# Performance work log

Hardware: AMD Instinct MI355X
Metric: run time of the kernel (lower is better)

The kernel has to match this reference:

```python
import jax, jax.numpy as jnp
import numpy as np

B, S, D, H, E, F, K = 4, 1024, 1024, 16, 8, 4096, 2
HD = D // H  # 64
EPS = 1e-6


def _rmsnorm(x, w):
    return x * jax.lax.rsqrt(jnp.mean(x * x, axis=-1, keepdims=True) + EPS) * w


def _rope(x, cos, sin):
    # x: [B,S,H,HD]; cos/sin: [S,HD//2]
    b, s, h, hd = x.shape
    x2 = x.reshape(b, s, h, hd // 2, 2)
    xr, xi = x2[..., 0], x2[..., 1]
    c = cos[None, :, None, :]
    sn = sin[None, :, None, :]
    or_ = xr * c - xi * sn
    oi = xr * sn + xi * c
    return jnp.stack([or_, oi], axis=-1).reshape(b, s, h, hd)


def setup_inputs() -> dict:
    key = jax.random.key(0)
    ks = jax.random.split(key, 16)
    sc = 0.02
    # rotary tables (standard LLaMa rope)
    inv = 1.0 / (10000.0 ** (np.arange(0, HD, 2, dtype=np.float32) / HD))
    ang = np.outer(np.arange(S, dtype=np.float32), inv)
    return {
        "q": jax.random.normal(ks[0], (B, S, D), jnp.float32),
        "k": jax.random.normal(ks[1], (B, S, D), jnp.float32),
        "v": jax.random.normal(ks[2], (B, S, D), jnp.float32),
        "freqs_cos": jnp.asarray(np.cos(ang)),
        "freqs_sin": jnp.asarray(np.sin(ang)),
        "att_norm_w": jnp.ones((D,), jnp.float32),
        "ffn_norm_w": jnp.ones((D,), jnp.float32),
        "wq": jax.random.normal(ks[3], (D, D), jnp.float32) * sc,
        "wk": jax.random.normal(ks[4], (D, D), jnp.float32) * sc,
        "wv": jax.random.normal(ks[5], (D, D), jnp.float32) * sc,
        "wo": jax.random.normal(ks[6], (D, D), jnp.float32) * sc,
        "router_w": jax.random.normal(ks[7], (E, D), jnp.float32) * sc,
        "router_b": jnp.zeros((E,), jnp.float32),
        "w1": jax.random.normal(ks[8], (E, F, D), jnp.float32) * sc,
        "w2": jax.random.normal(ks[9], (E, D, F), jnp.float32) * sc,
        "w3": jax.random.normal(ks[10], (E, F, D), jnp.float32) * sc,
        "is_causal": 1,
    }


def _attention(qn, kn, vn, freqs_cos, freqs_sin, wq, wk, wv, wo, is_causal):
    b, s, d = qn.shape
    qh = (qn @ wq.T).reshape(b, s, H, HD)
    kh = (kn @ wk.T).reshape(b, s, H, HD)
    vh = (vn @ wv.T).reshape(b, s, H, HD)
    qh = _rope(qh, freqs_cos, freqs_sin)
    kh = _rope(kh, freqs_cos, freqs_sin)
    scores = jnp.einsum("bqhd,bkhd->bhqk", qh, kh) / jnp.sqrt(jnp.float32(HD))
    if is_causal:
        causal = jnp.tril(jnp.ones((s, s), bool))
        scores = jnp.where(causal[None, None], scores, jnp.float32(-1e30))
    probs = jax.nn.softmax(scores, axis=-1)
    out = jnp.einsum("bhqk,bkhd->bqhd", probs, vh).reshape(b, s, d)
    return out @ wo.T


def _sparse_moe(x, router_w, router_b, w1, w2, w3):
    # x: [B,S,D]
    flat = x.reshape(-1, x.shape[-1])  # [T,D]
    logits = flat @ router_w.T + router_b  # [T,E]
    top_v, top_i = jax.lax.top_k(logits, K)  # eval mode: no noise
    probs = jax.nn.softmax(top_v, axis=-1)  # softmax over -inf-filled == softmax over top-k
    gates = jnp.sum(jax.nn.one_hot(top_i, E, dtype=flat.dtype) * probs[..., None], axis=1)  # [T,E]
    y = jnp.zeros_like(flat)
    for e in range(E):  # fixed small expert loop; gate==0 for unselected tokens (faithful to masked dispatch)
        hgate = jax.nn.silu(flat @ w1[e].T) * (flat @ w3[e].T)  # SwiGLU FFN_LLaMa
        y = y + gates[:, e : e + 1] * (hgate @ w2[e].T)
    return y.reshape(x.shape)


def reference(q, k, v, freqs_cos, freqs_sin, att_norm_w, ffn_norm_w, wq, wk, wv, wo,
              router_w, router_b, w1, w2, w3, is_causal):
    qn = _rmsnorm(q, att_norm_w)
    # self-attention path: k = v = normed q (q.clone())
    h = q + _attention(qn, qn, qn, freqs_cos, freqs_sin, wq, wk, wv, wo, is_causal)
    out = h + _sparse_moe(_rmsnorm(h, ffn_norm_w), router_w, router_b, w1, w2, w3)
    return out
```

## Files before the change

kernel.cpp:

```cpp
#include <hip/hip_runtime.h>
#include <hip/hip_bf16.h>
#include <math.h>

#define NB 4
#define SQ 1024
#define DM 1024
#define NH 16
#define HDm 64
#define NE 8
#define FFd 4096
#define NTOK 4096
#define RTOT 9216
#define EPSF 1e-6f

typedef __attribute__((ext_vector_type(8))) short bf16x8_t;
typedef __attribute__((ext_vector_type(4))) float f32x4_t;
typedef const __attribute__((address_space(1))) void* gas_t;
typedef __attribute__((address_space(3))) void* las_t;

__device__ __forceinline__ float b2f(unsigned short u){
  return __uint_as_float(((unsigned int)u) << 16);
}
__device__ __forceinline__ unsigned short f2b(float f){
  __hip_bfloat16 h = __float2bfloat16(f);
  unsigned short u;
  __builtin_memcpy(&u, &h, 2);
  return u;
}

__global__ __launch_bounds__(256) void convert_k(const float* __restrict__ s,
                                                 unsigned short* __restrict__ d, int n4){
  int i = blockIdx.x*256 + threadIdx.x;
  if (i >= n4) return;
  float4 v = ((const float4*)s)[i];
  ushort4 o; o.x=f2b(v.x); o.y=f2b(v.y); o.z=f2b(v.z); o.w=f2b(v.w);
  ((ushort4*)d)[i] = o;
}

__global__ __launch_bounds__(256) void split_k(const float* __restrict__ s,
                                               unsigned short* __restrict__ hi,
                                               unsigned short* __restrict__ lo, int n4){
  int i = blockIdx.x*256 + threadIdx.x;
  if (i >= n4) return;
  float4 v = ((const float4*)s)[i];
  ushort4 h, l;
  h.x=f2b(v.x); l.x=f2b(v.x - b2f(h.x));
  h.y=f2b(v.y); l.y=f2b(v.y - b2f(h.y));
  h.z=f2b(v.z); l.z=f2b(v.z - b2f(h.z));
  h.w=f2b(v.w); l.w=f2b(v.w - b2f(h.w));
  ((ushort4*)hi)[i] = h;
  ((ushort4*)lo)[i] = l;
}

__global__ __launch_bounds__(256) void rmsnorm_k(const float* __restrict__ x,
                                                 const float* __restrict__ w,
                                                 float* __restrict__ o){
  int row = blockIdx.x; int t = threadIdx.x;
  float4 v = ((const float4*)(x + (size_t)row*DM))[t];
  float ss = v.x*v.x + v.y*v.y + v.z*v.z + v.w*v.w;
  #pragma unroll
  for (int d=32; d; d>>=1) ss += __shfl_down(ss, d, 64);
  __shared__ float red[4];
  int wid = t>>6, ln = t&63;
  if (ln==0) red[wid] = ss;
  __syncthreads();
  float tot = red[0]+red[1]+red[2]+red[3];
  float sc = 1.0f/sqrtf(tot*(1.0f/DM) + EPSF);
  float4 wv = ((const float4*)w)[t];
  float4 ov = { v.x*sc*wv.x, v.y*sc*wv.y, v.z*sc*wv.z, v.w*sc*wv.w };
  ((float4*)(o + (size_t)row*DM))[t] = ov;
}

__global__ __launch_bounds__(256) void rmsnorm_split_k(const float* __restrict__ x,
                                                       const float* __restrict__ w,
                                                       unsigned short* __restrict__ hi,
                                                       unsigned short* __restrict__ lo){
  int row = blockIdx.x; int t = threadIdx.x;
  float4 v = ((const float4*)(x + (size_t)row*DM))[t];
  float ss = v.x*v.x + v.y*v.y + v.z*v.z + v.w*v.w;
  #pragma unroll
  for (int d=32; d; d>>=1) ss += __shfl_down(ss, d, 64);
  __shared__ float red[4];
  int wid = t>>6, ln = t&63;
  if (ln==0) red[wid] = ss;
  __syncthreads();
  float tot = red[0]+red[1]+red[2]+red[3];
  float sc = 1.0f/sqrtf(tot*(1.0f/DM) + EPSF);
  float4 wv = ((const float4*)w)[t];
  float4 ov = { v.x*sc*wv.x, v.y*sc*wv.y, v.z*sc*wv.z, v.w*sc*wv.w };
  ushort4 h, l;
  h.x=f2b(ov.x); l.x=f2b(ov.x - b2f(h.x));
  h.y=f2b(ov.y); l.y=f2b(ov.y - b2f(h.y));
  h.z=f2b(ov.z); l.z=f2b(ov.z - b2f(h.z));
  h.w=f2b(ov.w); l.w=f2b(ov.w - b2f(h.w));
  ((ushort4*)(hi + (size_t)row*DM))[t] = h;
  ((ushort4*)(lo + (size_t)row*DM))[t] = l;
}

__global__ __launch_bounds__(256) void gemm_nt_split(
  const unsigned short* __restrict__ Ah, const unsigned short* __restrict__ Al,
  const unsigned short* __restrict__ Bh0, const unsigned short* __restrict__ Bl0,
  const unsigned short* __restrict__ Bh1, const unsigned short* __restrict__ Bl1,
  const unsigned short* __restrict__ Bh2, const unsigned short* __restrict__ Bl2,
  float* __restrict__ C0, float* __restrict__ C1, float* __restrict__ C2,
  const float* __restrict__ resid, int Kd, int Ncols)
{
  const unsigned short* Bh = (blockIdx.z==0)?Bh0:(blockIdx.z==1)?Bh1:Bh2;
  const unsigned short* Bl = (blockIdx.z==0)?Bl0:(blockIdx.z==1)?Bl1:Bl2;
  float* C = (blockIdx.z==0)?C0:(blockIdx.z==1)?C1:C2;
  __shared__ unsigned short AsH[128*32];
  __shared__ unsigned short AsL[128*32];
  __shared__ unsigned short BsH[128*32];
  __shared__ unsigned short BsL[128*32];
  const int t = threadIdx.x;
  const int w = t>>6, lane = t&63;
  const int wm = w>>1, wn = w&1;
  const int lm = lane&15, fk = (lane>>4)*8;
  const int row0 = blockIdx.y*128, col0 = blockIdx.x*128;
  f32x4_t acc[4][4];
  #pragma unroll
  for (int i=0;i<4;i++)
    #pragma unroll
    for (int j=0;j<4;j++){ f32x4_t z = {0.f,0.f,0.f,0.f}; acc[i][j]=z; }
  for (int k0=0;k0<Kd;k0+=32){
    __syncthreads();
    #pragma unroll
    for (int j=0;j<2;j++){
      const int chunk = j*4 + w;
      const int gt = chunk*64 + lane;
      const int rw_ = gt>>2, kp = (gt&3)*8;
      const size_t aoff = (size_t)(row0+rw_)*Kd + k0 + kp;
      const size_t boff = (size_t)(col0+rw_)*Kd + k0 + kp;
      __builtin_amdgcn_global_load_lds((gas_t)(Ah + aoff), (las_t)(AsH + chunk*512), 16, 0, 0);
      __builtin_amdgcn_global_load_lds((gas_t)(Al + aoff), (las_t)(AsL + chunk*512), 16, 0, 0);
      __builtin_amdgcn_global_load_lds((gas_t)(Bh + boff), (las_t)(BsH + chunk*512), 16, 0, 0);
      __builtin_amdgcn_global_load_lds((gas_t)(Bl + boff), (las_t)(BsL + chunk*512), 16, 0, 0);
    }
    __syncthreads();
    bf16x8_t ah[4], al[4], bh[4], bl[4];
    #pragma unroll
    for (int f=0;f<4;f++){
      const size_t ao = (size_t)(wm*64 + f*16 + lm)*32 + fk;
      const size_t bo = (size_t)(wn*64 + f*16 + lm)*32 + fk;
      ah[f] = *(const bf16x8_t*)(AsH + ao);
      al[f] = *(const bf16x8_t*)(AsL + ao);
      bh[f] = *(const bf16x8_t*)(BsH + bo);
      bl[f] = *(const bf16x8_t*)(BsL + bo);
    }
    #pragma unroll
    for (int i=0;i<4;i++)
      #pragma unroll
      for (int j=0;j<4;j++){
        acc[i][j] = __builtin_amdgcn_mfma_f32_16x16x32_bf16(ah[i], bh[j], acc[i][j], 0, 0, 0);
        acc[i][j] = __builtin_amdgcn_mfma_f32_16x16x32_bf16(al[i], bh[j], acc[i][j], 0, 0, 0);
        acc[i][j] = __builtin_amdgcn_mfma_f32_16x16x32_bf16(ah[i], bl[j], acc[i][j], 0, 0, 0);
      }
  }
  const int rbase = row0 + wm*64 + (lane>>4)*4;
  const int cbase = col0 + wn*64 + lm;
  #pragma unroll
  for (int i=0;i<4;i++)
    #pragma unroll
    for (int j=0;j<4;j++)
      #pragma unroll
      for (int r=0;r<4;r++){
        const size_t idx = (size_t)(rbase + i*16 + r)*Ncols + cbase + j*16;
        float v = acc[i][j][r];
        if (resid) v += resid[idx];
        C[idx] = v;
      }
}

__global__ __launch_bounds__(256) void rope_k(float* __restrict__ qh, float* __restrict__ kh,
  const float* __restrict__ fc, const float* __restrict__ fs){
  int idx = blockIdx.x*256 + threadIdx.x;
  if (idx >= NTOK*NH*32) return;
  int i = idx & 31;
  int h = (idx>>5) & (NH-1);
  int n = idx >> 9;
  int s = n & (SQ-1);
  float c = fc[s*32+i], sn = fs[s*32+i];
  size_t base = (size_t)n*DM + h*HDm + 2*i;
  float xr = qh[base], xi = qh[base+1];
  qh[base]   = xr*c - xi*sn;
  qh[base+1] = xr*sn + xi*c;
  xr = kh[base]; xi = kh[base+1];
  kh[base]   = xr*c - xi*sn;
  kh[base+1] = xr*sn + xi*c;
}

__global__ __launch_bounds__(256) void flash_k(
  const float* __restrict__ qh, const float* __restrict__ kh, const float* __restrict__ vh,
  float* __restrict__ ctx, const int* __restrict__ causp)
{
  __shared__ float Qt[64][68];
  __shared__ float KP[64][68];
  __shared__ float Vs[64][68];
  __shared__ float red[64][17];
  __shared__ float mrow[64], lrow[64], arow[64];
  const int qt = blockIdx.x;
  const int b = blockIdx.y >> 4, h = blockIdx.y & 15;
  const int t = threadIdx.x;
  const int row = t>>2, cb = (t&3)*16;
  const int ty = t>>4, tx = t&15;
  const size_t headoff = ((size_t)b*SQ)*DM + (size_t)h*HDm;
  const int q0 = qt*64;
  {
    const float* qp = qh + headoff + (size_t)(q0+row)*DM + cb;
    #pragma unroll
    for (int j=0;j<4;j++){
      float4 v = *(const float4*)(qp + 4*j);
      Qt[cb+4*j+0][row]=v.x; Qt[cb+4*j+1][row]=v.y; Qt[cb+4*j+2][row]=v.z; Qt[cb+4*j+3][row]=v.w;
    }
  }
  if (t<64){ mrow[t]=-1e30f; lrow[t]=0.f; }
  float O[4][4] = {};
  const int causal = *causp;
  const int ktmax = causal ? qt : (SQ/64 - 1);
  for (int kt=0; kt<=ktmax; ++kt){
    const int k0 = kt*64;
    __syncthreads();
    {
      const float* kp_ = kh + headoff + (size_t)(k0+row)*DM + cb;
      const float* vp_ = vh + headoff + (size_t)(k0+row)*DM + cb;
      #pragma unroll
      for (int j=0;j<4;j++){
        float4 v = *(const float4*)(kp_ + 4*j);
        KP[cb+4*j+0][row]=v.x; KP[cb+4*j+1][row]=v.y; KP[cb+4*j+2][row]=v.z; KP[cb+4*j+3][row]=v.w;
        float4 u = *(const float4*)(vp_ + 4*j);
        *(float4*)&Vs[row][cb+4*j] = u;
      }
    }
    __syncthreads();
    float Sv[4][4] = {};
    #pragma unroll 16
    for (int kk=0;kk<64;kk++){
      float4 qa = *(const float4*)&Qt[kk][ty*4];
      float4 kb = *(const float4*)&KP[kk][tx*4];
      float a4[4]={qa.x,qa.y,qa.z,qa.w}, b4[4]={kb.x,kb.y,kb.z,kb.w};
      #pragma unroll
      for (int i=0;i<4;i++)
        #pragma unroll
        for (int j=0;j<4;j++)
          Sv[i][j] = fmaf(a4[i], b4[j], Sv[i][j]);
    }
    #pragma unroll
    for (int i=0;i<4;i++){
      float lm = -3.0e30f;
      #pragma unroll
      for (int j=0;j<4;j++){
        float s = Sv[i][j]*0.125f;
        if (causal && (k0+tx*4+j) > (q0+ty*4+i)) s = -1e30f;
        Sv[i][j] = s;
        lm = fmaxf(lm, s);
      }
      red[ty*4+i][tx] = lm;
    }
    __syncthreads();
    if (t<64){
      float m = red[t][0];
      #pragma unroll
      for (int j=1;j<16;j++) m = fmaxf(m, red[t][j]);
      float mo = mrow[t];
      float mn = fmaxf(mo, m);
      float al = expf(mo - mn);
      mrow[t]=mn; arow[t]=al; lrow[t]*=al;
    }
    __syncthreads();
    #pragma unroll
    for (int i=0;i<4;i++){
      int r = ty*4+i;
      float mn = mrow[r];
      float rs = 0.f;
      #pragma unroll
      for (int j=0;j<4;j++){
        float p = expf(Sv[i][j]-mn);
        KP[tx*4+j][r] = p;
        rs += p;
      }
      red[r][tx] = rs;
    }
    __syncthreads();
    if (t<64){
      float s_=0.f;
      #pragma unroll
      for (int j=0;j<16;j++) s_ += red[t][j];
      lrow[t] += s_;
    }
    #pragma unroll
    for (int i=0;i<4;i++){
      float al = arow[ty*4+i];
      #pragma unroll
      for (int j=0;j<4;j++) O[i][j]*=al;
    }
    #pragma unroll 16
    for (int kk=0;kk<64;kk++){
      float4 pa = *(const float4*)&KP[kk][ty*4];
      float4 vb = *(const float4*)&Vs[kk][tx*4];
      float a4[4]={pa.x,pa.y,pa.z,pa.w}, b4[4]={vb.x,vb.y,vb.z,vb.w};
      #pragma unroll
      for (int i=0;i<4;i++)
        #pragma unroll
        for (int j=0;j<4;j++)
          O[i][j] = fmaf(a4[i], b4[j], O[i][j]);
    }
  }
  __syncthreads();
  #pragma unroll
  for (int i=0;i<4;i++){
    float il = 1.0f/lrow[ty*4+i];
    float4 ov = { O[i][0]*il, O[i][1]*il, O[i][2]*il, O[i][3]*il };
    *(float4*)(ctx + headoff + (size_t)(q0+ty*4+i)*DM + tx*4) = ov;
  }
}

__global__ __launch_bounds__(256) void router_k(
  const float* __restrict__ hn, const float* __restrict__ rw, const float* __restrict__ rb,
  int* __restrict__ topi, float* __restrict__ topp, int* __restrict__ counts)
{
  const int n = blockIdx.x, t = threadIdx.x;
  float4 x = ((const float4*)(hn + (size_t)n*DM))[t];
  float p[NE];
  #pragma unroll
  for (int e=0;e<NE;e++){
    float4 wv = ((const float4*)(rw + (size_t)e*DM))[t];
    p[e] = x.x*wv.x + x.y*wv.y + x.z*wv.z + x.w*wv.w;
  }
  #pragma unroll
  for (int e=0;e<NE;e++)
    #pragma unroll
    for (int d=32; d; d>>=1) p[e] += __shfl_down(p[e], d, 64);
  __shared__ float red[4][NE];
  int wid=t>>6, ln=t&63;
  if (ln==0){
    #pragma unroll
    for (int e=0;e<NE;e++) red[wid][e]=p[e];
  }
  __syncthreads();
  if (t==0){
    float v1=-3e30f, v2=-3e30f; int i1=0, i2=0;
    for (int e=0;e<NE;e++){
      float v = red[0][e]+red[1][e]+red[2][e]+red[3][e]+rb[e];
      if (v > v1){ v2=v1;i2=i1; v1=v;i1=e; }
      else if (v > v2){ v2=v;i2=e; }
    }
    float ex = expf(v2-v1);
    float g1 = 1.0f/(1.0f+ex);
    float g2 = ex*g1;
    topi[2*n]=i1; topi[2*n+1]=i2;
    topp[2*n]=g1; topp[2*n+1]=g2;
    atomicAdd(&counts[i1],1); atomicAdd(&counts[i2],1);
  }
}

__global__ void offsets_k(const int* __restrict__ counts, int* __restrict__ offs){
  if (blockIdx.x==0 && threadIdx.x==0){
    int run=0;
    for (int e=0;e<NE;e++){ offs[e]=run; run += (counts[e]+127)&~127; }
    offs[NE]=run;
  }
}

__global__ __launch_bounds__(256) void assign_k(const int* __restrict__ topi,
  const int* __restrict__ offs, int* __restrict__ cursor,
  int* __restrict__ list, int* __restrict__ inv){
  int t = blockIdx.x*256 + threadIdx.x;
  if (t >= NTOK*2) return;
  int e = topi[t];
  int slot = atomicAdd(&cursor[e], 1);
  int pos = offs[e] + slot;
  list[pos] = t>>1;
  inv[t] = pos;
}

__global__ __launch_bounds__(256) void gather_k(const float* __restrict__ hn,
  const int* __restrict__ offs, const int* __restrict__ counts, const int* __restrict__ list,
  unsigned short* __restrict__ xg){
  const int p = blockIdx.x;
  if (p >= offs[NE]) return;
  int e=0;
  while (offs[e+1] <= p) ++e;
  const int t = threadIdx.x;
  ushort4 o;
  if (p - offs[e] < counts[e]){
    int n = list[p];
    float4 x = ((const float4*)(hn + (size_t)n*DM))[t];
    o.x=f2b(x.x); o.y=f2b(x.y); o.z=f2b(x.z); o.w=f2b(x.w);
  } else { o.x=0; o.y=0; o.z=0; o.w=0; }
  ((ushort4*)(xg + (size_t)p*DM))[t] = o;
}

__global__ __launch_bounds__(256) void gemm_moe_bf16(
  const unsigned short* __restrict__ Aall, const unsigned short* __restrict__ Wall,
  unsigned short* __restrict__ Call, const int* __restrict__ offs, int Kd, int Ncols)
{
  const int row0 = blockIdx.y*128;
  if (row0 >= offs[NE]) return;
  int e=0;
  while (offs[e+1] <= row0) ++e;
  const unsigned short* Wp = Wall + (size_t)e*Ncols*Kd;
  const int col0 = blockIdx.x*128;
  __shared__ unsigned short As[128*32];
  __shared__ unsigned short Bs[128*32];
  const int t = threadIdx.x;
  const int w = t>>6, lane = t&63;
  const int wm = w>>1, wn = w&1;
  const int lm = lane&15, fk = (lane>>4)*8;
  f32x4_t acc[4][4];
  #pragma unroll
  for (int i=0;i<4;i++)
    #pragma unroll
    for (int j=0;j<4;j++){ f32x4_t z = {0.f,0.f,0.f,0.f}; acc[i][j]=z; }
  for (int k0=0;k0<Kd;k0+=32){
    __syncthreads();
    #pragma unroll
    for (int j=0;j<2;j++){
      const int chunk = j*4 + w;
      const int gt = chunk*64 + lane;
      const int rw_ = gt>>2, kp = (gt&3)*8;
      __builtin_amdgcn_global_load_lds((gas_t)(Aall + (size_t)(row0+rw_)*Kd + k0 + kp),
                                       (las_t)(As + chunk*512), 16, 0, 0);
      __builtin_amdgcn_global_load_lds((gas_t)(Wp + (size_t)(col0+rw_)*Kd + k0 + kp),
                                       (las_t)(Bs + chunk*512), 16, 0, 0);
    }
    __syncthreads();
    bf16x8_t af[4], bfr[4];
    #pragma unroll
    for (int f=0;f<4;f++){
      af[f]  = *(const bf16x8_t*)(As + (size_t)(wm*64 + f*16 + lm)*32 + fk);
      bfr[f] = *(const bf16x8_t*)(Bs + (size_t)(wn*64 + f*16 + lm)*32 + fk);
    }
    #pragma unroll
    for (int i=0;i<4;i++)
      #pragma unroll
      for (int j=0;j<4;j++)
        acc[i][j] = __builtin_amdgcn_mfma_f32_16x16x32_bf16(af[i], bfr[j], acc[i][j], 0, 0, 0);
  }
  const int rbase = row0 + wm*64 + (lane>>4)*4;
  const int cbase = col0 + wn*64 + lm;
  #pragma unroll
  for (int i=0;i<4;i++)
    #pragma unroll
    for (int j=0;j<4;j++)
      #pragma unroll
      for (int r=0;r<4;r++)
        Call[(size_t)(rbase + i*16 + r)*Ncols + cbase + j*16] = f2b(acc[i][j][r]);
}

__global__ __launch_bounds__(256) void silu_mul_k(unsigned short* __restrict__ h1,
                                                  const unsigned short* __restrict__ h3){
  size_t i = (size_t)blockIdx.x*256 + threadIdx.x;
  ushort4 a = ((const ushort4*)h1)[i];
  ushort4 b = ((const ushort4*)h3)[i];
  ushort4 o;
  float fa, fb, s_;
  fa=b2f(a.x); fb=b2f(b.x); s_=fa/(1.f+__expf(-fa)); o.x=f2b(s_*fb);
  fa=b2f(a.y); fb=b2f(b.y); s_=fa/(1.f+__expf(-fa)); o.y=f2b(s_*fb);
  fa=b2f(a.z); fb=b2f(b.z); s_=fa/(1.f+__expf(-fa)); o.z=f2b(s_*fb);
  fa=b2f(a.w); fb=b2f(b.w); s_=fa/(1.f+__expf(-fa)); o.w=f2b(s_*fb);
  ((ushort4*)h1)[i] = o;
}

__global__ __launch_bounds__(256) void combine_k(const float* __restrict__ h,
  const unsigned short* __restrict__ yb, const float* __restrict__ topp,
  const int* __restrict__ inv, float* __restrict__ out)
{
  const int n = blockIdx.x, t = threadIdx.x;
  const int p0 = inv[2*n], p1 = inv[2*n+1];
  const float g0 = topp[2*n], g1 = topp[2*n+1];
  float4 hv = ((const float4*)(h + (size_t)n*DM))[t];
  ushort4 y0 = ((const ushort4*)(yb + (size_t)p0*DM))[t];
  ushort4 y1 = ((const ushort4*)(yb + (size_t)p1*DM))[t];
  float4 ov;
  ov.x = hv.x + g0*b2f(y0.x) + g1*b2f(y1.x);
  ov.y = hv.y + g0*b2f(y0.y) + g1*b2f(y1.y);
  ov.z = hv.z + g0*b2f(y0.z) + g1*b2f(y1.z);
  ov.w = hv.w + g0*b2f(y0.w) + g1*b2f(y1.w);
  ((float4*)(out + (size_t)n*DM))[t] = ov;
}

extern "C" void kernel_launch(void* const* d_in, const int* in_sizes, int n_in,
                              void* d_out, int out_size, void* d_ws, size_t ws_size,
                              hipStream_t stream)
{
  (void)in_sizes; (void)n_in; (void)out_size; (void)ws_size;
  const float* q    = (const float*)d_in[0];
  const float* fc   = (const float*)d_in[3];
  const float* fs   = (const float*)d_in[4];
  const float* attw = (const float*)d_in[5];
  const float* ffnw = (const float*)d_in[6];
  const float* wq   = (const float*)d_in[7];
  const float* wk   = (const float*)d_in[8];
  const float* wv   = (const float*)d_in[9];
  const float* wo   = (const float*)d_in[10];
  const float* rw   = (const float*)d_in[11];
  const float* rb   = (const float*)d_in[12];
  const float* w1   = (const float*)d_in[13];
  const float* w2   = (const float*)d_in[14];
  const float* w3   = (const float*)d_in[15];
  const int*   caus = (const int*)d_in[16];
  float* out = (float*)d_out;

  char* ws = (char*)d_ws;
  size_t off = 0;
  auto take = [&](size_t bytes)->char*{ char* r = ws + off; off += (bytes + 255) & ~(size_t)255; return r; };
  unsigned short* qnh = (unsigned short*)take((size_t)NTOK*DM*2);
  unsigned short* qnl = (unsigned short*)take((size_t)NTOK*DM*2);
  float* qh   = (float*)take((size_t)NTOK*DM*4);
  float* kh   = (float*)take((size_t)NTOK*DM*4);
  float* vh   = (float*)take((size_t)NTOK*DM*4);
  float* hbuf = (float*)take((size_t)NTOK*DM*4);
  unsigned short* h1  = (unsigned short*)take((size_t)RTOT*FFd*2);
  unsigned short* h3  = (unsigned short*)take((size_t)RTOT*FFd*2);
  unsigned short* yb  = (unsigned short*)take((size_t)RTOT*DM*2);
  unsigned short* w1b = (unsigned short*)take((size_t)NE*FFd*DM*2);
  unsigned short* w3b = (unsigned short*)take((size_t)NE*FFd*DM*2);
  unsigned short* w2b = (unsigned short*)take((size_t)NE*FFd*DM*2);
  int*   counts = (int*)take(64);
  int*   cursor = counts + 8;
  int*   offs   = (int*)take(64);
  int*   topi   = (int*)take((size_t)NTOK*2*4);
  float* topp   = (float*)take((size_t)NTOK*2*4);
  int*   list   = (int*)take((size_t)RTOT*4);
  int*   inv    = (int*)take((size_t)NTOK*2*4);

  float* ctx = (float*)qnh;
  unsigned short* ctxh = (unsigned short*)qh;
  unsigned short* ctxl = ctxh + (size_t)NTOK*DM;
  float* hn = kh;
  unsigned short* xg = yb;
  unsigned short* wqh = (unsigned short*)h1;
  unsigned short* wql = wqh + (size_t)DM*DM;
  unsigned short* wkh = wql + (size_t)DM*DM;
  unsigned short* wkl = wkh + (size_t)DM*DM;
  unsigned short* wvh = wkl + (size_t)DM*DM;
  unsigned short* wvl = wvh + (size_t)DM*DM;
  unsigned short* woh = wvl + (size_t)DM*DM;
  unsigned short* wol = woh + (size_t)DM*DM;

  const int nw4 = NE*FFd*DM/4;
  convert_k<<<nw4/256, 256, 0, stream>>>(w1, w1b, nw4);
  convert_k<<<nw4/256, 256, 0, stream>>>(w3, w3b, nw4);
  convert_k<<<nw4/256, 256, 0, stream>>>(w2, w2b, nw4);

  const int nwq4 = DM*DM/4;
  split_k<<<nwq4/256, 256, 0, stream>>>(wq, wqh, wql, nwq4);
  split_k<<<nwq4/256, 256, 0, stream>>>(wk, wkh, wkl, nwq4);
  split_k<<<nwq4/256, 256, 0, stream>>>(wv, wvh, wvl, nwq4);
  split_k<<<nwq4/256, 256, 0, stream>>>(wo, woh, wol, nwq4);

  rmsnorm_split_k<<<NTOK, 256, 0, stream>>>(q, attw, qnh, qnl);
  gemm_nt_split<<<dim3(8,32,3), 256, 0, stream>>>(qnh, qnl,
      wqh, wql, wkh, wkl, wvh, wvl, qh, kh, vh, nullptr, DM, DM);
  rope_k<<<NTOK*NH*32/256, 256, 0, stream>>>(qh, kh, fc, fs);
  flash_k<<<dim3(SQ/64, NB*NH), 256, 0, stream>>>(qh, kh, vh, ctx, caus);
  split_k<<<NTOK*DM/4/256, 256, 0, stream>>>(ctx, ctxh, ctxl, NTOK*DM/4);
  gemm_nt_split<<<dim3(8,32,1), 256, 0, stream>>>(ctxh, ctxl,
      woh, wol, woh, wol, woh, wol, hbuf, hbuf, hbuf, q, DM, DM);
  rmsnorm_k<<<NTOK, 256, 0, stream>>>(hbuf, ffnw, hn);

  hipMemsetAsync(counts, 0, 64, stream);
  router_k<<<NTOK, 256, 0, stream>>>(hn, rw, rb, topi, topp, counts);
  offsets_k<<<1, 64, 0, stream>>>(counts, offs);
  assign_k<<<NTOK*2/256, 256, 0, stream>>>(topi, offs, cursor, list, inv);
  gather_k<<<RTOT, 256, 0, stream>>>(hn, offs, counts, list, xg);

  gemm_moe_bf16<<<dim3(FFd/128, RTOT/128), 256, 0, stream>>>(xg, w1b, h1, offs, DM, FFd);
  gemm_moe_bf16<<<dim3(FFd/128, RTOT/128), 256, 0, stream>>>(xg, w3b, h3, offs, DM, FFd);
  silu_mul_k<<<RTOT*FFd/4/256, 256, 0, stream>>>(h1, h3);
  gemm_moe_bf16<<<dim3(DM/128, RTOT/128), 256, 0, stream>>>(h1, w2b, yb, offs, FFd, DM);
  combine_k<<<NTOK, 256, 0, stream>>>(hbuf, yb, topp, inv, out);
}
```

Before: 1.415 ms.

## Rewrite flash attention with bf16 MFMA and fuse split into epilogue

Replaces the scalar fp32 flash-attention kernel with a bf16 MFMA version. RoPE now writes pre-scaled bf16 Q and K, and a new kernel transposes V into bf16. The attention kernel loads tiles into LDS with global_load_lds, keeps softmax stats in registers with lane shuffles instead of shared-memory reductions, and writes the hi/lo bf16 split of ctx directly, so the separate split kernel is removed. This trades fp32 attention accuracy for bf16 inputs and P, and adds an extra V transpose pass.

```diff
diff --git a/kernel.cpp b/kernel.cpp
--- a/kernel.cpp
+++ b/kernel.cpp
@@ -171,8 +171,9 @@
       }
 }
 
-__global__ __launch_bounds__(256) void rope_k(float* __restrict__ qh, float* __restrict__ kh,
-  const float* __restrict__ fc, const float* __restrict__ fs){
+__global__ __launch_bounds__(256) void rope_bf16_k(const float* __restrict__ qh,
+  const float* __restrict__ kh, const float* __restrict__ fc, const float* __restrict__ fs,
+  unsigned short* __restrict__ qb, unsigned short* __restrict__ kb){
   int idx = blockIdx.x*256 + threadIdx.x;
   if (idx >= NTOK*NH*32) return;
   int i = idx & 31;
@@ -182,135 +183,170 @@
   float c = fc[s*32+i], sn = fs[s*32+i];
   size_t base = (size_t)n*DM + h*HDm + 2*i;
   float xr = qh[base], xi = qh[base+1];
-  qh[base]   = xr*c - xi*sn;
-  qh[base+1] = xr*sn + xi*c;
+  float or_ = (xr*c - xi*sn) * 0.125f;
+  float oi  = (xr*sn + xi*c) * 0.125f;
+  unsigned int pq = (unsigned int)f2b(or_) | ((unsigned int)f2b(oi) << 16);
+  *(unsigned int*)(qb + base) = pq;
   xr = kh[base]; xi = kh[base+1];
-  kh[base]   = xr*c - xi*sn;
-  kh[base+1] = xr*sn + xi*c;
-}
-
-__global__ __launch_bounds__(256) void flash_k(
-  const float* __restrict__ qh, const float* __restrict__ kh, const float* __restrict__ vh,
-  float* __restrict__ ctx, const int* __restrict__ causp)
+  or_ = xr*c - xi*sn; oi = xr*sn + xi*c;
+  unsigned int pk = (unsigned int)f2b(or_) | ((unsigned int)f2b(oi) << 16);
+  *(unsigned int*)(kb + base) = pk;
+}
+
+__global__ __launch_bounds__(256) void vtrans_k(const float* __restrict__ vh,
+                                                unsigned short* __restrict__ vT){
+  __shared__ unsigned short Lt[64][72];
+  const int st = blockIdx.x, bh = blockIdx.y;
+  const int b = bh >> 4, h = bh & 15;
+  const int t = threadIdx.x;
+  const int s0 = st*64;
+  const int sr = t >> 2, hq = (t & 3) * 16;
+  const float* src = vh + ((size_t)(b*SQ + s0 + sr))*DM + h*HDm + hq;
+  #pragma unroll
+  for (int i=0;i<4;i++){
+    float4 v = *(const float4*)(src + 4*i);
+    Lt[hq+4*i+0][sr] = f2b(v.x);
+    Lt[hq+4*i+1][sr] = f2b(v.y);
+    Lt[hq+4*i+2][sr] = f2b(v.z);
+    Lt[hq+4*i+3][sr] = f2b(v.w);
+  }
+  __syncthreads();
+  const int hd = t >> 2, sq = (t & 3) * 16;
+  unsigned short* dst = vT + ((size_t)bh*HDm + hd)*SQ + s0 + sq;
+  #pragma unroll
+  for (int i=0;i<2;i++){
+    bf16x8_t x = *(const bf16x8_t*)&Lt[hd][sq + 8*i];
+    *(bf16x8_t*)(dst + 8*i) = x;
+  }
+}
+
+__global__ __launch_bounds__(256) void flash_mfma_k(
+  const unsigned short* __restrict__ qb, const unsigned short* __restrict__ kb,
+  const unsigned short* __restrict__ vT,
+  unsigned short* __restrict__ ctxh, unsigned short* __restrict__ ctxl,
+  const int* __restrict__ causp)
 {
-  __shared__ float Qt[64][68];
-  __shared__ float KP[64][68];
-  __shared__ float Vs[64][68];
-  __shared__ float red[64][17];
-  __shared__ float mrow[64], lrow[64], arow[64];
+  __shared__ unsigned short Qs[2*64*32];
+  __shared__ unsigned short Ks[2*64*32];
+  __shared__ unsigned short Vt[2*64*32];
+  __shared__ unsigned short Ps[2*64*32];
   const int qt = blockIdx.x;
-  const int b = blockIdx.y >> 4, h = blockIdx.y & 15;
+  const int bh = blockIdx.y;
+  const int b = bh >> 4, h = bh & 15;
   const int t = threadIdx.x;
-  const int row = t>>2, cb = (t&3)*16;
-  const int ty = t>>4, tx = t&15;
-  const size_t headoff = ((size_t)b*SQ)*DM + (size_t)h*HDm;
-  const int q0 = qt*64;
-  {
-    const float* qp = qh + headoff + (size_t)(q0+row)*DM + cb;
-    #pragma unroll
-    for (int j=0;j<4;j++){
-      float4 v = *(const float4*)(qp + 4*j);
-      Qt[cb+4*j+0][row]=v.x; Qt[cb+4*j+1][row]=v.y; Qt[cb+4*j+2][row]=v.z; Qt[cb+4*j+3][row]=v.w;
-    }
-  }
-  if (t<64){ mrow[t]=-1e30f; lrow[t]=0.f; }
-  float O[4][4] = {};
+  const int w = t >> 6, lane = t & 63;
+  const int lm = lane & 15, g = lane >> 4, fk = g * 8;
+  const int q0 = qt * 64;
+  const size_t qkoff = (size_t)b * SQ * DM + (size_t)h * HDm;
+  const size_t voff  = ((size_t)bh * HDm) * SQ;
+
+  #pragma unroll
+  for (int j=0;j<2;j++){
+    const int s = j*4 + w;
+    const int c = s >> 2, r0 = (s & 3) * 16;
+    const int row = r0 + (lane >> 2), kp = (lane & 3) * 8;
+    __builtin_amdgcn_global_load_lds((gas_t)(qb + qkoff + (size_t)(q0+row)*DM + c*32 + kp),
+                                     (las_t)(Qs + s*512), 16, 0, 0);
+  }
+  __syncthreads();
+  bf16x8_t aq0 = *(const bf16x8_t*)(Qs + 0*2048 + (w*16+lm)*32 + fk);
+  bf16x8_t aq1 = *(const bf16x8_t*)(Qs + 1*2048 + (w*16+lm)*32 + fk);
+
   const int causal = *causp;
   const int ktmax = causal ? qt : (SQ/64 - 1);
+  f32x4_t O[4];
+  #pragma unroll
+  for (int j=0;j<4;j++){ f32x4_t z={0.f,0.f,0.f,0.f}; O[j]=z; }
+  float mrow[4], lrow[4];
+  #pragma unroll
+  for (int r=0;r<4;r++){ mrow[r] = -3e30f; lrow[r] = 0.f; }
+
   for (int kt=0; kt<=ktmax; ++kt){
     const int k0 = kt*64;
     __syncthreads();
-    {
-      const float* kp_ = kh + headoff + (size_t)(k0+row)*DM + cb;
-      const float* vp_ = vh + headoff + (size_t)(k0+row)*DM + cb;
+    #pragma unroll
+    for (int j=0;j<2;j++){
+      const int s = j*4 + w;
+      const int c = s >> 2, r0 = (s & 3) * 16;
+      const int row = r0 + (lane >> 2), kp = (lane & 3) * 8;
+      __builtin_amdgcn_global_load_lds((gas_t)(kb + qkoff + (size_t)(k0+row)*DM + c*32 + kp),
+                                       (las_t)(Ks + s*512), 16, 0, 0);
+      __builtin_amdgcn_global_load_lds((gas_t)(vT + voff + (size_t)row*SQ + k0 + c*32 + kp),
+                                       (las_t)(Vt + s*512), 16, 0, 0);
+    }
+    __syncthreads();
+
+    f32x4_t Sv[4];
+    #pragma unroll
+    for (int j=0;j<4;j++){ f32x4_t z={0.f,0.f,0.f,0.f}; Sv[j]=z; }
+    #pragma unroll
+    for (int j=0;j<4;j++){
+      bf16x8_t b0 = *(const bf16x8_t*)(Ks + 0*2048 + (j*16+lm)*32 + fk);
+      bf16x8_t b1 = *(const bf16x8_t*)(Ks + 1*2048 + (j*16+lm)*32 + fk);
+      Sv[j] = __builtin_amdgcn_mfma_f32_16x16x32_bf16(aq0, b0, Sv[j], 0, 0, 0);
+      Sv[j] = __builtin_amdgcn_mfma_f32_16x16x32_bf16(aq1, b1, Sv[j], 0, 0, 0);
+    }
+    const int rowq = q0 + w*16 + g*4;
+    if (causal && kt == qt){
       #pragma unroll
       for (int j=0;j<4;j++){
-        float4 v = *(const float4*)(kp_ + 4*j);
-        KP[cb+4*j+0][row]=v.x; KP[cb+4*j+1][row]=v.y; KP[cb+4*j+2][row]=v.z; KP[cb+4*j+3][row]=v.w;
-        float4 u = *(const float4*)(vp_ + 4*j);
-        *(float4*)&Vs[row][cb+4*j] = u;
+        const int col = k0 + j*16 + lm;
+        #pragma unroll
+        for (int r=0;r<4;r++)
+          if (col > rowq + r) Sv[j][r] = -3e30f;
       }
     }
-    __syncthreads();
-    float Sv[4][4] = {};
-    #pragma unroll 16
-    for (int kk=0;kk<64;kk++){
-      float4 qa = *(const float4*)&Qt[kk][ty*4];
-      float4 kb = *(const float4*)&KP[kk][tx*4];
-      float a4[4]={qa.x,qa.y,qa.z,qa.w}, b4[4]={kb.x,kb.y,kb.z,kb.w};
-      #pragma unroll
-      for (int i=0;i<4;i++)
-        #pragma unroll
-        for (int j=0;j<4;j++)
-          Sv[i][j] = fmaf(a4[i], b4[j], Sv[i][j]);
-    }
-    #pragma unroll
-    for (int i=0;i<4;i++){
-      float lm = -3.0e30f;
+    float alpha[4];
+    #pragma unroll
+    for (int r=0;r<4;r++){
+      float m_ = fmaxf(fmaxf(Sv[0][r],Sv[1][r]), fmaxf(Sv[2][r],Sv[3][r]));
+      #pragma unroll
+      for (int d=1; d<16; d<<=1) m_ = fmaxf(m_, __shfl_xor(m_, d, 64));
+      const float mn = fmaxf(mrow[r], m_);
+      alpha[r] = __expf(mrow[r] - mn);
+      mrow[r] = mn;
+    }
+    #pragma unroll
+    for (int r=0;r<4;r++){
+      const int qrow = w*16 + g*4 + r;
+      float rs = 0.f;
       #pragma unroll
       for (int j=0;j<4;j++){
-        float s = Sv[i][j]*0.125f;
-        if (causal && (k0+tx*4+j) > (q0+ty*4+i)) s = -1e30f;
-        Sv[i][j] = s;
-        lm = fmaxf(lm, s);
+        const float p = __expf(Sv[j][r] - mrow[r]);
+        rs += p;
+        const int key5 = (((j&1)<<4) | lm) ^ (g<<3);
+        Ps[(j>>1)*2048 + qrow*32 + key5] = f2b(p);
       }
-      red[ty*4+i][tx] = lm;
-    }
-    __syncthreads();
-    if (t<64){
-      float m = red[t][0];
-      #pragma unroll
-      for (int j=1;j<16;j++) m = fmaxf(m, red[t][j]);
-      float mo = mrow[t];
-      float mn = fmaxf(mo, m);
-      float al = expf(mo - mn);
-      mrow[t]=mn; arow[t]=al; lrow[t]*=al;
-    }
-    __syncthreads();
-    #pragma unroll
-    for (int i=0;i<4;i++){
-      int r = ty*4+i;
-      float mn = mrow[r];
-      float rs = 0.f;
-      #pragma unroll
-      for (int j=0;j<4;j++){
-        float p = expf(Sv[i][j]-mn);
-        KP[tx*4+j][r] = p;
-        rs += p;
-      }
-      red[r][tx] = rs;
-    }
-    __syncthreads();
-    if (t<64){
-      float s_=0.f;
-      #pragma unroll
-      for (int j=0;j<16;j++) s_ += red[t][j];
-      lrow[t] += s_;
-    }
-    #pragma unroll
-    for (int i=0;i<4;i++){
-      float al = arow[ty*4+i];
-      #pragma unroll
-      for (int j=0;j<4;j++) O[i][j]*=al;
-    }
-    #pragma unroll 16
-    for (int kk=0;kk<64;kk++){
-      float4 pa = *(const float4*)&KP[kk][ty*4];
-      float4 vb = *(const float4*)&Vs[kk][tx*4];
-      float a4[4]={pa.x,pa.y,pa.z,pa.w}, b4[4]={vb.x,vb.y,vb.z,vb.w};
-      #pragma unroll
-      for (int i=0;i<4;i++)
-        #pragma unroll
-        for (int j=0;j<4;j++)
-          O[i][j] = fmaf(a4[i], b4[j], O[i][j]);
-    }
-  }
-  __syncthreads();
-  #pragma unroll
-  for (int i=0;i<4;i++){
-    float il = 1.0f/lrow[ty*4+i];
-    float4 ov = { O[i][0]*il, O[i][1]*il, O[i][2]*il, O[i][3]*il };
-    *(float4*)(ctx + headoff + (size_t)(q0+ty*4+i)*DM + tx*4) = ov;
+      #pragma unroll
+      for (int d=1; d<16; d<<=1) rs += __shfl_xor(rs, d, 64);
+      lrow[r] = lrow[r]*alpha[r] + rs;
+      #pragma unroll
+      for (int j=0;j<4;j++) O[j][r] *= alpha[r];
+    }
+    const int fkp = fk ^ (((lm>>2)&3)<<3);
+    bf16x8_t pa0 = *(const bf16x8_t*)(Ps + 0*2048 + (w*16+lm)*32 + fkp);
+    bf16x8_t pa1 = *(const bf16x8_t*)(Ps + 1*2048 + (w*16+lm)*32 + fkp);
+    #pragma unroll
+    for (int j=0;j<4;j++){
+      bf16x8_t v0 = *(const bf16x8_t*)(Vt + 0*2048 + (j*16+lm)*32 + fk);
+      bf16x8_t v1 = *(const bf16x8_t*)(Vt + 1*2048 + (j*16+lm)*32 + fk);
+      O[j] = __builtin_amdgcn_mfma_f32_16x16x32_bf16(pa0, v0, O[j], 0, 0, 0);
+      O[j] = __builtin_amdgcn_mfma_f32_16x16x32_bf16(pa1, v1, O[j], 0, 0, 0);
+    }
+  }
+  #pragma unroll
+  for (int r=0;r<4;r++){
+    const float il = 1.0f / lrow[r];
+    const size_t rowtok = (size_t)(q0 + w*16 + g*4 + r);
+    #pragma unroll
+    for (int j=0;j<4;j++){
+      const float v = O[j][r] * il;
+      const unsigned short hi = f2b(v);
+      const float lo = v - b2f(hi);
+      const size_t idx = qkoff + rowtok*DM + j*16 + lm;
+      ctxh[idx] = hi;
+      ctxl[idx] = f2b(lo);
+    }
   }
 }
 
@@ -524,9 +560,8 @@
   int*   list   = (int*)take((size_t)RTOT*4);
   int*   inv    = (int*)take((size_t)NTOK*2*4);
 
-  float* ctx = (float*)qnh;
-  unsigned short* ctxh = (unsigned short*)qh;
-  unsigned short* ctxl = ctxh + (size_t)NTOK*DM;
+  unsigned short* ctxh = qnh;
+  unsigned short* ctxl = qnl;
   float* hn = kh;
   unsigned short* xg = yb;
   unsigned short* wqh = (unsigned short*)h1;
@@ -537,6 +572,9 @@
   unsigned short* wvl = wvh + (size_t)DM*DM;
   unsigned short* woh = wvl + (size_t)DM*DM;
   unsigned short* wol = woh + (size_t)DM*DM;
+  unsigned short* qb  = wqh + 8*(size_t)DM*DM;
+  unsigned short* kb  = qb + (size_t)NTOK*DM;
+  unsigned short* vTb = (unsigned short*)h3;
 
   const int nw4 = NE*FFd*DM/4;
   convert_k<<<nw4/256, 256, 0, stream>>>(w1, w1b, nw4);
@@ -552,9 +590,9 @@
   rmsnorm_split_k<<<NTOK, 256, 0, stream>>>(q, attw, qnh, qnl);
   gemm_nt_split<<<dim3(8,32,3), 256, 0, stream>>>(qnh, qnl,
       wqh, wql, wkh, wkl, wvh, wvl, qh, kh, vh, nullptr, DM, DM);
-  rope_k<<<NTOK*NH*32/256, 256, 0, stream>>>(qh, kh, fc, fs);
-  flash_k<<<dim3(SQ/64, NB*NH), 256, 0, stream>>>(qh, kh, vh, ctx, caus);
-  split_k<<<NTOK*DM/4/256, 256, 0, stream>>>(ctx, ctxh, ctxl, NTOK*DM/4);
+  rope_bf16_k<<<NTOK*NH*32/256, 256, 0, stream>>>(qh, kh, fc, fs, qb, kb);
+  vtrans_k<<<dim3(SQ/64, NB*NH), 256, 0, stream>>>(vh, vTb);
+  flash_mfma_k<<<dim3(SQ/64, NB*NH), 256, 0, stream>>>(qb, kb, vTb, ctxh, ctxl, caus);
   gemm_nt_split<<<dim3(8,32,1), 256, 0, stream>>>(ctxh, ctxl,
       woh, wol, woh, wol, woh, wol, hbuf, hbuf, hbuf, q, DM, DM);
   rmsnorm_k<<<NTOK, 256, 0, stream>>>(hbuf, ffnw, hn);
```

Result: faster. 1.219 ms (-13.9%).
